# Optimization experiments

Hardware: AMD Instinct MI355X
Metric: run time of the kernel (lower is better)

## Reference

```python
import jax, jax.numpy as jnp
import numpy as np

LOG_2PI = float(np.log(2.0 * np.pi))
LOSS_BETA = 1.0
SIGMA = 1.0
EPS = 1e-6


def setup_inputs() -> dict:
    key = jax.random.key(0)
    z_activations = jax.random.normal(key, (2048, 16, 8), dtype=jnp.float32)
    return {"z_activations": z_activations}


def reference(z_activations):
    N, num_attr, pose_dim = z_activations.shape
    x = z_activations.reshape(N, -1)  # (N, K)
    K = x.shape[1]

    # standardize (torch.std is unbiased, ddof=1)
    mean = jnp.mean(x, axis=0, keepdims=True)
    std = jnp.std(x, axis=0, keepdims=True, ddof=1)
    x = (x - mean) / (std + EPS)

    logN = jnp.log(jnp.asarray(N, dtype=x.dtype))

    # per-dimension pairwise squared differences: (N, N, K)
    d = (x[:, None, :] - x[None, :, :]) ** 2

    # joint: log p(x_i | x_j) for K-dim Gaussian, sigma=1
    sq_dist = jnp.sum(d, axis=2)  # (N, N)
    c_joint = -0.5 * K * LOG_2PI - K * jnp.log(jnp.asarray(SIGMA, dtype=x.dtype))
    log_prob_joint = c_joint - sq_dist / (2.0 * SIGMA ** 2)
    log_q_z_given_x = jax.nn.logsumexp(log_prob_joint, axis=1) - logN  # (N,)

    # marginals: 1-D Gaussian per dim, all K at once (fuses the torch K-loop)
    c_marg = -0.5 * LOG_2PI - jnp.log(jnp.asarray(SIGMA, dtype=x.dtype))
    log_prob_marg = c_marg - d / (2.0 * SIGMA ** 2)  # (N, N, K)
    log_q_z_j = jax.nn.logsumexp(log_prob_marg, axis=1) - logN  # (N, K)
    sum_log_q_z_j = jnp.sum(log_q_z_j, axis=1)  # (N,)

    tc_loss = jnp.mean(log_q_z_given_x - sum_log_q_z_j)
    return tc_loss * LOSS_BETA
```

## Files before the change

### kernel.cpp

```cpp
#include <hip/hip_runtime.h>

#define NROWS 2048
#define KDIM  128
#define TJ    64
#define NCELL 16
#define PORD  10

typedef float v4f __attribute__((ext_vector_type(4)));

__device__ __forceinline__ float fexp2(float x){ return __builtin_amdgcn_exp2f(x); }
__device__ __forceinline__ float flog2(float x){ return __builtin_amdgcn_logf(x); }

#define CS 0.8493218002880191f

template<int CTRL>
__device__ __forceinline__ float dpp_ror(float v){
  int r = __builtin_amdgcn_update_dpp(0, __builtin_bit_cast(int, v), CTRL, 0xF, 0xF, true);
  return __builtin_bit_cast(float, r);
}

__device__ __forceinline__ void col_stats(const float* __restrict__ accum, int k,
                                          float& scale, float& shift){
  float s = accum[k], s2 = accum[KDIM + k];
  float m = s * (1.f / NROWS);
  float var = fmaxf((s2 - (float)NROWS * m * m) * (1.f / (NROWS - 1)), 0.f);
  scale = 1.f / (sqrtf(var) + 1e-6f);
  shift = -m * scale;
}

__device__ __forceinline__ void quad_stats(const float* __restrict__ accum, int q,
                                           float4& sc, float4& sh){
  const float4 s  = reinterpret_cast<const float4*>(accum)[q];
  const float4 s2 = reinterpret_cast<const float4*>(accum + KDIM)[q];
  const float invN = 1.f / NROWS, invN1 = 1.f / (NROWS - 1);
#define COMP(c) { float m = s.c * invN; \
                  float var = fmaxf((s2.c - (float)NROWS * m * m) * invN1, 0.f); \
                  float sca = CS / (sqrtf(var) + 1e-6f); sc.c = sca; sh.c = -m * sca; }
  COMP(x) COMP(y) COMP(z) COMP(w)
#undef COMP
}

__global__ __launch_bounds__(1024) void tc_stats(const float* __restrict__ x,
                                                 float* __restrict__ accum){
  const int t  = threadIdx.x;
  const int k  = t & 127;
  const int rg = t >> 7;
  const int r0 = blockIdx.x * 64;
  float s = 0.f, s2 = 0.f;
  #pragma unroll
  for (int it = 0; it < 8; ++it){
    float v = x[(size_t)(r0 + it * 8 + rg) * KDIM + k];
    s += v;
    s2 = fmaf(v, v, s2);
  }
  __shared__ float ls[8][128], ls2[8][128];
  ls[rg][k] = s; ls2[rg][k] = s2;
  __syncthreads();
  if (t < 128){
    float a = 0.f, b = 0.f;
    #pragma unroll
    for (int g = 0; g < 8; ++g){ a += ls[g][t]; b += ls2[g][t]; }
    atomicAdd(&accum[t], a);
    atomicAdd(&accum[128 + t], b);
  }
}

__global__ __launch_bounds__(128) void tc_moments(const float* __restrict__ x,
                                                  const float* __restrict__ accum,
                                                  float* __restrict__ mom2){
  const int k   = blockIdx.x >> 4;
  const int seg = blockIdx.x & 15;
  const int t   = threadIdx.x;
  __shared__ float lm[NCELL * PORD];
  lm[t] = 0.f;
  if (t < 32) lm[128 + t] = 0.f;
  __syncthreads();

  float scale, shift; col_stats(accum, k, scale, shift);
  const int row = seg * 128 + t;
  float y = fmaf(x[(size_t)row * KDIM + k], scale, shift);
  int c = (int)floorf(y * 2.f + 8.f);
  c = min(max(c, 0), NCELL - 1);
  float u = y - (-3.75f + 0.5f * (float)c);
  float* b10 = &lm[c * PORD];
  atomicAdd(&b10[0], 1.f);
  float pw = u;
  atomicAdd(&b10[1], pw);
  pw *= u; atomicAdd(&b10[2], pw * 0.5f);
  pw *= u; atomicAdd(&b10[3], pw * 1.6666666666e-1f);
  pw *= u; atomicAdd(&b10[4], pw * 4.1666666666e-2f);
  pw *= u; atomicAdd(&b10[5], pw * 8.3333333333e-3f);
  pw *= u; atomicAdd(&b10[6], pw * 1.3888888889e-3f);
  pw *= u; atomicAdd(&b10[7], pw * 1.9841269841e-4f);
  pw *= u; atomicAdd(&b10[8], pw * 2.4801587302e-5f);
  pw *= u; atomicAdd(&b10[9], pw * 2.7557319224e-6f);
  __syncthreads();

  for (int idx = t; idx < NCELL * PORD; idx += 128){
    int c2 = idx / PORD, m = idx - c2 * PORD;
    atomicAdd(&mom2[(size_t)(c2 * KDIM + k) * 12 + m], lm[idx]);
  }
}

__global__ __launch_bounds__(256) void tc_eval(const float* __restrict__ x,
                                               const float* __restrict__ accum,
                                               const float* __restrict__ mom2,
                                               float* __restrict__ slog){
  const int t   = threadIdx.x;
  const int k   = t & 127;
  const int ir  = t >> 7;
  const int row = blockIdx.x * 2 + ir;
  float scale, shift; col_stats(accum, k, scale, shift);
  const float y = fmaf(x[(size_t)row * KDIM + k], scale, shift);

  float S = 0.f;
  #pragma unroll
  for (int c = 0; c < NCELL; ++c){
    const float* mp = mom2 + (size_t)(c * KDIM + k) * 12;
    float4 q0 = *reinterpret_cast<const float4*>(mp);
    float4 q1 = *reinterpret_cast<const float4*>(mp + 4);
    float4 q2 = *reinterpret_cast<const float4*>(mp + 8);
    float s  = y - (-3.75f + 0.5f * (float)c);
    float sc = s * CS;
    float e  = fexp2(-(sc * sc));
    float prev = 1.f, cur = s, nxt;
    float inner = fmaf(q0.y, s, q0.x);
    nxt = fmaf(s, cur, -prev);        inner = fmaf(q0.z, nxt, inner); prev = cur; cur = nxt;
    nxt = fmaf(s, cur, -2.f * prev);  inner = fmaf(q0.w, nxt, inner); prev = cur; cur = nxt;
    nxt = fmaf(s, cur, -3.f * prev);  inner = fmaf(q1.x, nxt, inner); prev = cur; cur = nxt;
    nxt = fmaf(s, cur, -4.f * prev);  inner = fmaf(q1.y, nxt, inner); prev = cur; cur = nxt;
    nxt = fmaf(s, cur, -5.f * prev);  inner = fmaf(q1.z, nxt, inner); prev = cur; cur = nxt;
    nxt = fmaf(s, cur, -6.f * prev);  inner = fmaf(q1.w, nxt, inner); prev = cur; cur = nxt;
    nxt = fmaf(s, cur, -7.f * prev);  inner = fmaf(q2.x, nxt, inner); prev = cur; cur = nxt;
    nxt = fmaf(s, cur, -8.f * prev);  inner = fmaf(q2.y, nxt, inner);
    S = fmaf(e, inner, S);
  }
  float lg = flog2(S);
  #pragma unroll
  for (int off = 1; off < 64; off <<= 1) lg += __shfl_xor(lg, off);
  if ((t & 63) == 0) atomicAdd(&slog[row], lg);
}

__global__ __launch_bounds__(512) void tc_joint(const float* __restrict__ x,
                                                const float* __restrict__ accum,
                                                float* __restrict__ joint){
  __shared__ float tile[TJ][KDIM];
  const int t    = threadIdx.x;
  const int wave = t >> 6;
  const int lane = t & 63;
  const int g    = lane >> 4;
  const int h    = lane & 15;
  const int row  = blockIdx.x * 32 + wave * 4 + g;
  const int jbase = blockIdx.y * 256;

  const int kq = t & 31;
  float4 sc4, sh4; quad_stats(accum, kq, sc4, sh4);

  v4f xA, xB;
  {
    float4 scA, shA, scB, shB;
    quad_stats(accum, h,      scA, shA);
    quad_stats(accum, 16 + h, scB, shB);
    float4 rA = reinterpret_cast<const float4*>(x + (size_t)row * KDIM)[h];
    float4 rB = reinterpret_cast<const float4*>(x + (size_t)row * KDIM)[16 + h];
    xA = (v4f){fmaf(rA.x, scA.x, shA.x), fmaf(rA.y, scA.y, shA.y),
               fmaf(rA.z, scA.z, shA.z), fmaf(rA.w, scA.w, shA.w)};
    xB = (v4f){fmaf(rB.x, scB.x, shB.x), fmaf(rB.y, scB.y, shB.y),
               fmaf(rB.z, scB.z, shB.z), fmaf(rB.w, scB.w, shB.w)};
  }

  float jacc = 0.f;
  const int jr0 = t >> 5;

  for (int jt = 0; jt < 256; jt += TJ){
    __syncthreads();
    #pragma unroll
    for (int p = 0; p < 4; ++p){
      const int jr = jr0 + 16 * p;
      float4 v = reinterpret_cast<const float4*>(x + (size_t)(jbase + jt + jr) * KDIM)[kq];
      v4f w = {fmaf(v.x, sc4.x, sh4.x), fmaf(v.y, sc4.y, sh4.y),
               fmaf(v.z, sc4.z, sh4.z), fmaf(v.w, sc4.w, sh4.w)};
      *reinterpret_cast<v4f*>(&tile[jr][kq * 4]) = w;
    }
    __syncthreads();

    #pragma unroll 8
    for (int j = 0; j < TJ; ++j){
      const v4f a = *reinterpret_cast<const v4f*>(&tile[j][4 * h]);
      const v4f b = *reinterpret_cast<const v4f*>(&tile[j][64 + 4 * h]);
      v4f uA = xA - a, uB = xB - b;
      float pd = uA.x * uA.x;
      pd = fmaf(uA.y, uA.y, pd); pd = fmaf(uA.z, uA.z, pd); pd = fmaf(uA.w, uA.w, pd);
      pd = fmaf(uB.x, uB.x, pd); pd = fmaf(uB.y, uB.y, pd);
      pd = fmaf(uB.z, uB.z, pd); pd = fmaf(uB.w, uB.w, pd);
      pd += dpp_ror<0x121>(pd);
      pd += dpp_ror<0x122>(pd);
      pd += dpp_ror<0x124>(pd);
      pd += dpp_ror<0x128>(pd);
      if (__ballot(pd < 65.f)) jacc += fexp2(-pd);
    }
  }
  if (h == 0) atomicAdd(&joint[row], jacc);
}

__global__ __launch_bounds__(256) void tc_final(const float* __restrict__ joint,
                                                const float* __restrict__ slog,
                                                float* __restrict__ out){
  const int r = blockIdx.x * 256 + threadIdx.x;
  float vi = 0.6931471805599453f * (flog2(joint[r]) - slog[r]) + 968.32661124224364f;
  #pragma unroll
  for (int off = 32; off > 0; off >>= 1) vi += __shfl_down(vi, off);
  __shared__ float rs[4];
  const int wave = threadIdx.x >> 6, lane = threadIdx.x & 63;
  if (lane == 0) rs[wave] = vi;
  __syncthreads();
  if (threadIdx.x == 0){
    float tot = rs[0] + rs[1] + rs[2] + rs[3];
    atomicAdd(out, tot * (1.0f / NROWS));
  }
}

extern "C" void kernel_launch(void* const* d_in, const int* in_sizes, int n_in,
                              void* d_out, int out_size, void* d_ws, size_t ws_size,
                              hipStream_t stream){
  const float* x = (const float*)d_in[0];
  float* out   = (float*)d_out;
  float* wsf   = (float*)d_ws;
  float* accum = wsf;
  float* joint = wsf + 256;
  float* slog  = wsf + 256 + 2048;
  float* mom2  = wsf + 256 + 4096;
  const size_t ws_floats = 256 + 4096 + 24576;
  (void)hipMemsetAsync(wsf, 0, ws_floats * sizeof(float), stream);
  (void)hipMemsetAsync(d_out, 0, sizeof(float), stream);

  tc_stats  <<<32, 1024, 0, stream>>>(x, accum);
  tc_moments<<<KDIM * 16, 128, 0, stream>>>(x, accum, mom2);
  tc_joint  <<<dim3(64, 8), 512, 0, stream>>>(x, accum, joint);
  tc_eval   <<<NROWS / 2, 256, 0, stream>>>(x, accum, mom2, slog);
  tc_final  <<<NROWS / 256, 256, 0, stream>>>(joint, slog, out);
}
```

Baseline: 131.9 us.

## Exploit pairwise symmetry in joint kernel and fuse eval/final into it

The joint kernel now visits only the upper-triangular 256x256 block pairs. Off-diagonal tiles also add their exponentials into the column rows through shared-memory atomics, which roughly halves the pairwise work. The marginal-evaluation and final-reduction kernels are folded into the joint kernel, and a last-block counter performs the final sum. The two memsets are replaced by zeroing inside tc_stats, and the global atomics for column stats become per-block partials that tc_moments reduces. The costs are extra shared atomics in the hot loop, load imbalance between diagonal and off-diagonal blocks, and a fixed-order serial tail.

```diff
diff --git a/kernel.cpp b/kernel.cpp
--- a/kernel.cpp
+++ b/kernel.cpp
@@ -5,6 +5,7 @@
 #define TJ    64
 #define NCELL 16
 #define PORD  10
+#define NJBLK 576
 
 typedef float v4f __attribute__((ext_vector_type(4)));
 
@@ -19,9 +20,16 @@
   return __builtin_bit_cast(float, r);
 }
 
-__device__ __forceinline__ void col_stats(const float* __restrict__ accum, int k,
-                                          float& scale, float& shift){
-  float s = accum[k], s2 = accum[KDIM + k];
+#define OFF_PART   0
+#define OFF_ACCUM  8192
+#define OFF_JOINT  8448
+#define OFF_SLOG   10496
+#define OFF_MOM    12544
+#define OFF_CTR    33024
+#define ZERO_BASE  OFF_JOINT
+#define ZERO_LEN   (2048 + 2048 + 20480 + 4)
+
+__device__ __forceinline__ void col_stats_from(float s, float s2, float& scale, float& shift){
   float m = s * (1.f / NROWS);
   float var = fmaxf((s2 - (float)NROWS * m * m) * (1.f / (NROWS - 1)), 0.f);
   scale = 1.f / (sqrtf(var) + 1e-6f);
@@ -41,11 +49,15 @@
 }
 
 __global__ __launch_bounds__(1024) void tc_stats(const float* __restrict__ x,
-                                                 float* __restrict__ accum){
+                                                 float* __restrict__ ws){
   const int t  = threadIdx.x;
   const int k  = t & 127;
   const int rg = t >> 7;
   const int r0 = blockIdx.x * 64;
+  {
+    int idx = blockIdx.x * 1024 + t;
+    if (idx < ZERO_LEN) ws[ZERO_BASE + idx] = 0.f;
+  }
   float s = 0.f, s2 = 0.f;
   #pragma unroll
   for (int it = 0; it < 8; ++it){
@@ -60,23 +72,33 @@
     float a = 0.f, b = 0.f;
     #pragma unroll
     for (int g = 0; g < 8; ++g){ a += ls[g][t]; b += ls2[g][t]; }
-    atomicAdd(&accum[t], a);
-    atomicAdd(&accum[128 + t], b);
+    ws[OFF_PART + blockIdx.x * 256 + t]       = a;
+    ws[OFF_PART + blockIdx.x * 256 + 128 + t] = b;
   }
 }
 
 __global__ __launch_bounds__(128) void tc_moments(const float* __restrict__ x,
-                                                  const float* __restrict__ accum,
-                                                  float* __restrict__ mom2){
+                                                  float* __restrict__ ws){
   const int k   = blockIdx.x >> 4;
   const int seg = blockIdx.x & 15;
   const int t   = threadIdx.x;
   __shared__ float lm[NCELL * PORD];
   lm[t] = 0.f;
   if (t < 32) lm[128 + t] = 0.f;
-  __syncthreads();
-
-  float scale, shift; col_stats(accum, k, scale, shift);
+
+  float s = 0.f, s2 = 0.f;
+  #pragma unroll
+  for (int b = 0; b < 32; ++b){
+    s  += ws[OFF_PART + b * 256 + k];
+    s2 += ws[OFF_PART + b * 256 + 128 + k];
+  }
+  if (seg == 0 && t == 0){
+    ws[OFF_ACCUM + k]       = s;
+    ws[OFF_ACCUM + 128 + k] = s2;
+  }
+  float scale, shift; col_stats_from(s, s2, scale, shift);
+  __syncthreads();
+
   const int row = seg * 128 + t;
   float y = fmaf(x[(size_t)row * KDIM + k], scale, shift);
   int c = (int)floorf(y * 2.f + 8.f);
@@ -96,62 +118,42 @@
   pw *= u; atomicAdd(&b10[9], pw * 2.7557319224e-6f);
   __syncthreads();
 
+  float* mom = ws + OFF_MOM;
   for (int idx = t; idx < NCELL * PORD; idx += 128){
     int c2 = idx / PORD, m = idx - c2 * PORD;
-    atomicAdd(&mom2[(size_t)(c2 * KDIM + k) * 12 + m], lm[idx]);
-  }
-}
-
-__global__ __launch_bounds__(256) void tc_eval(const float* __restrict__ x,
-                                               const float* __restrict__ accum,
-                                               const float* __restrict__ mom2,
-                                               float* __restrict__ slog){
-  const int t   = threadIdx.x;
-  const int k   = t & 127;
-  const int ir  = t >> 7;
-  const int row = blockIdx.x * 2 + ir;
-  float scale, shift; col_stats(accum, k, scale, shift);
-  const float y = fmaf(x[(size_t)row * KDIM + k], scale, shift);
-
-  float S = 0.f;
-  #pragma unroll
-  for (int c = 0; c < NCELL; ++c){
-    const float* mp = mom2 + (size_t)(c * KDIM + k) * 12;
-    float4 q0 = *reinterpret_cast<const float4*>(mp);
-    float4 q1 = *reinterpret_cast<const float4*>(mp + 4);
-    float4 q2 = *reinterpret_cast<const float4*>(mp + 8);
-    float s  = y - (-3.75f + 0.5f * (float)c);
-    float sc = s * CS;
-    float e  = fexp2(-(sc * sc));
-    float prev = 1.f, cur = s, nxt;
-    float inner = fmaf(q0.y, s, q0.x);
-    nxt = fmaf(s, cur, -prev);        inner = fmaf(q0.z, nxt, inner); prev = cur; cur = nxt;
-    nxt = fmaf(s, cur, -2.f * prev);  inner = fmaf(q0.w, nxt, inner); prev = cur; cur = nxt;
-    nxt = fmaf(s, cur, -3.f * prev);  inner = fmaf(q1.x, nxt, inner); prev = cur; cur = nxt;
-    nxt = fmaf(s, cur, -4.f * prev);  inner = fmaf(q1.y, nxt, inner); prev = cur; cur = nxt;
-    nxt = fmaf(s, cur, -5.f * prev);  inner = fmaf(q1.z, nxt, inner); prev = cur; cur = nxt;
-    nxt = fmaf(s, cur, -6.f * prev);  inner = fmaf(q1.w, nxt, inner); prev = cur; cur = nxt;
-    nxt = fmaf(s, cur, -7.f * prev);  inner = fmaf(q2.x, nxt, inner); prev = cur; cur = nxt;
-    nxt = fmaf(s, cur, -8.f * prev);  inner = fmaf(q2.y, nxt, inner);
-    S = fmaf(e, inner, S);
-  }
-  float lg = flog2(S);
-  #pragma unroll
-  for (int off = 1; off < 64; off <<= 1) lg += __shfl_xor(lg, off);
-  if ((t & 63) == 0) atomicAdd(&slog[row], lg);
+    atomicAdd(&mom[(size_t)(c2 * KDIM + k) * PORD + m], lm[idx]);
+  }
 }
 
 __global__ __launch_bounds__(512) void tc_joint(const float* __restrict__ x,
-                                                const float* __restrict__ accum,
-                                                float* __restrict__ joint){
+                                                float* __restrict__ ws,
+                                                float* __restrict__ out){
   __shared__ float tile[TJ][KDIM];
+  __shared__ float colacc[128];
+  __shared__ int   lastflag;
+  const float* accum = ws + OFF_ACCUM;
+  float* joint = ws + OFF_JOINT;
+  float* slog  = ws + OFF_SLOG;
+  const float* mom = ws + OFF_MOM;
+
+  const int bid  = blockIdx.x;
   const int t    = threadIdx.x;
   const int wave = t >> 6;
   const int lane = t & 63;
   const int g    = lane >> 4;
   const int h    = lane & 15;
-  const int row  = blockIdx.x * 32 + wave * 4 + g;
-  const int jbase = blockIdx.y * 256;
+
+  int pair = bid >> 4, sub = (bid >> 1) & 7, jhalf = bid & 1;
+  int a = 0, rem = pair;
+  while (rem >= 8 - a){ rem -= 8 - a; ++a; }
+  const int b = a + rem;
+  const int i0 = a * 256 + sub * 32;
+  const int j0 = b * 256 + jhalf * 128;
+  const bool offdiag = (a != b);
+
+  const int row = i0 + wave * 4 + g;
+
+  if (t < 128) colacc[t] = 0.f;
 
   const int kq = t & 31;
   float4 sc4, sh4; quad_stats(accum, kq, sc4, sh4);
@@ -172,12 +174,12 @@
   float jacc = 0.f;
   const int jr0 = t >> 5;
 
-  for (int jt = 0; jt < 256; jt += TJ){
+  for (int jt = 0; jt < 128; jt += TJ){
     __syncthreads();
     #pragma unroll
     for (int p = 0; p < 4; ++p){
       const int jr = jr0 + 16 * p;
-      float4 v = reinterpret_cast<const float4*>(x + (size_t)(jbase + jt + jr) * KDIM)[kq];
+      float4 v = reinterpret_cast<const float4*>(x + (size_t)(j0 + jt + jr) * KDIM)[kq];
       v4f w = {fmaf(v.x, sc4.x, sh4.x), fmaf(v.y, sc4.y, sh4.y),
                fmaf(v.z, sc4.z, sh4.z), fmaf(v.w, sc4.w, sh4.w)};
       *reinterpret_cast<v4f*>(&tile[jr][kq * 4]) = w;
@@ -186,37 +188,95 @@
 
     #pragma unroll 8
     for (int j = 0; j < TJ; ++j){
-      const v4f a = *reinterpret_cast<const v4f*>(&tile[j][4 * h]);
-      const v4f b = *reinterpret_cast<const v4f*>(&tile[j][64 + 4 * h]);
-      v4f uA = xA - a, uB = xB - b;
-      float pd = uA.x * uA.x;
-      pd = fmaf(uA.y, uA.y, pd); pd = fmaf(uA.z, uA.z, pd); pd = fmaf(uA.w, uA.w, pd);
-      pd = fmaf(uB.x, uB.x, pd); pd = fmaf(uB.y, uB.y, pd);
-      pd = fmaf(uB.z, uB.z, pd); pd = fmaf(uB.w, uB.w, pd);
+      const v4f aa = *reinterpret_cast<const v4f*>(&tile[j][4 * h]);
+      const v4f bb = *reinterpret_cast<const v4f*>(&tile[j][64 + 4 * h]);
+      v4f uA = xA - aa, uB = xB - bb;
+      float p0 = uA.x * uA.x, p1 = uA.y * uA.y;
+      p0 = fmaf(uA.z, uA.z, p0); p1 = fmaf(uA.w, uA.w, p1);
+      p0 = fmaf(uB.x, uB.x, p0); p1 = fmaf(uB.y, uB.y, p1);
+      p0 = fmaf(uB.z, uB.z, p0); p1 = fmaf(uB.w, uB.w, p1);
+      float pd = p0 + p1;
       pd += dpp_ror<0x121>(pd);
       pd += dpp_ror<0x122>(pd);
       pd += dpp_ror<0x124>(pd);
       pd += dpp_ror<0x128>(pd);
-      if (__ballot(pd < 65.f)) jacc += fexp2(-pd);
-    }
-  }
+      if (__ballot(pd < 65.f)){
+        float e = fexp2(-pd);
+        jacc += e;
+        if (offdiag && h == 0) atomicAdd(&colacc[jt + j], e);
+      }
+    }
+  }
+
   if (h == 0) atomicAdd(&joint[row], jacc);
-}
-
-__global__ __launch_bounds__(256) void tc_final(const float* __restrict__ joint,
-                                                const float* __restrict__ slog,
-                                                float* __restrict__ out){
-  const int r = blockIdx.x * 256 + threadIdx.x;
-  float vi = 0.6931471805599453f * (flog2(joint[r]) - slog[r]) + 968.32661124224364f;
-  #pragma unroll
-  for (int off = 32; off > 0; off >>= 1) vi += __shfl_down(vi, off);
-  __shared__ float rs[4];
-  const int wave = threadIdx.x >> 6, lane = threadIdx.x & 63;
-  if (lane == 0) rs[wave] = vi;
-  __syncthreads();
-  if (threadIdx.x == 0){
-    float tot = rs[0] + rs[1] + rs[2] + rs[3];
-    atomicAdd(out, tot * (1.0f / NROWS));
+  __syncthreads();
+  if (offdiag && t < 128){
+    float c = colacc[t];
+    if (c != 0.f) atomicAdd(&joint[j0 + t], c);
+  }
+
+  if (bid < 512){
+    const int k  = t & 127;
+    const int ir = t >> 7;
+    const int r  = bid * 4 + ir;
+    float scale, shift;
+    col_stats_from(accum[k], accum[128 + k], scale, shift);
+    const float y = fmaf(x[(size_t)r * KDIM + k], scale, shift);
+    float S = 0.f;
+    #pragma unroll
+    for (int c = 0; c < NCELL; ++c){
+      const float* mp = mom + (size_t)(c * KDIM + k) * PORD;
+      float q0 = mp[0], q1 = mp[1], q2 = mp[2], q3 = mp[3], q4 = mp[4];
+      float q5 = mp[5], q6 = mp[6], q7 = mp[7], q8 = mp[8], q9 = mp[9];
+      float s  = y - (-3.75f + 0.5f * (float)c);
+      float scl = s * CS;
+      float e  = fexp2(-(scl * scl));
+      float prev = 1.f, cur = s, nxt;
+      float inner = fmaf(q1, s, q0);
+      nxt = fmaf(s, cur, -prev);        inner = fmaf(q2, nxt, inner); prev = cur; cur = nxt;
+      nxt = fmaf(s, cur, -2.f * prev);  inner = fmaf(q3, nxt, inner); prev = cur; cur = nxt;
+      nxt = fmaf(s, cur, -3.f * prev);  inner = fmaf(q4, nxt, inner); prev = cur; cur = nxt;
+      nxt = fmaf(s, cur, -4.f * prev);  inner = fmaf(q5, nxt, inner); prev = cur; cur = nxt;
+      nxt = fmaf(s, cur, -5.f * prev);  inner = fmaf(q6, nxt, inner); prev = cur; cur = nxt;
+      nxt = fmaf(s, cur, -6.f * prev);  inner = fmaf(q7, nxt, inner); prev = cur; cur = nxt;
+      nxt = fmaf(s, cur, -7.f * prev);  inner = fmaf(q8, nxt, inner); prev = cur; cur = nxt;
+      nxt = fmaf(s, cur, -8.f * prev);  inner = fmaf(q9, nxt, inner);
+      S = fmaf(e, inner, S);
+    }
+    float lg = flog2(S);
+    #pragma unroll
+    for (int off = 1; off < 64; off <<= 1) lg += __shfl_xor(lg, off);
+    if (lane == 0) atomicAdd(&slog[r], lg);
+  }
+
+  __syncthreads();
+  if (t == 0){
+    __threadfence();
+    unsigned int* ctr = (unsigned int*)(ws + OFF_CTR);
+    unsigned int old = __hip_atomic_fetch_add(ctr, 1u, __ATOMIC_ACQ_REL, __HIP_MEMORY_SCOPE_AGENT);
+    lastflag = (old == NJBLK - 1);
+  }
+  __syncthreads();
+  if (lastflag){
+    __shared__ float red[8];
+    float acc = 0.f;
+    #pragma unroll
+    for (int q = 0; q < 4; ++q){
+      int r = q * 512 + t;
+      float jv = __hip_atomic_load(&joint[r], __ATOMIC_RELAXED, __HIP_MEMORY_SCOPE_AGENT);
+      float sv = __hip_atomic_load(&slog[r],  __ATOMIC_RELAXED, __HIP_MEMORY_SCOPE_AGENT);
+      acc += 0.6931471805599453f * (flog2(jv) - sv);
+    }
+    #pragma unroll
+    for (int off = 1; off < 64; off <<= 1) acc += __shfl_xor(acc, off);
+    if (lane == 0) red[wave] = acc;
+    __syncthreads();
+    if (t == 0){
+      float tot = 0.f;
+      #pragma unroll
+      for (int w2 = 0; w2 < 8; ++w2) tot += red[w2];
+      out[0] = tot * (1.0f / NROWS) + 968.32661124224364f;
+    }
   }
 }
 
@@ -224,19 +284,10 @@
                               void* d_out, int out_size, void* d_ws, size_t ws_size,
                               hipStream_t stream){
   const float* x = (const float*)d_in[0];
-  float* out   = (float*)d_out;
-  float* wsf   = (float*)d_ws;
-  float* accum = wsf;
-  float* joint = wsf + 256;
-  float* slog  = wsf + 256 + 2048;
-  float* mom2  = wsf + 256 + 4096;
-  const size_t ws_floats = 256 + 4096 + 24576;
-  (void)hipMemsetAsync(wsf, 0, ws_floats * sizeof(float), stream);
-  (void)hipMemsetAsync(d_out, 0, sizeof(float), stream);
-
-  tc_stats  <<<32, 1024, 0, stream>>>(x, accum);
-  tc_moments<<<KDIM * 16, 128, 0, stream>>>(x, accum, mom2);
-  tc_joint  <<<dim3(64, 8), 512, 0, stream>>>(x, accum, joint);
-  tc_eval   <<<NROWS / 2, 256, 0, stream>>>(x, accum, mom2, slog);
-  tc_final  <<<NROWS / 256, 256, 0, stream>>>(joint, slog, out);
-}
+  float* out = (float*)d_out;
+  float* ws  = (float*)d_ws;
+
+  tc_stats  <<<32, 1024, 0, stream>>>(x, ws);
+  tc_moments<<<KDIM * 16, 128, 0, stream>>>(x, ws);
+  tc_joint  <<<NJBLK, 512, 0, stream>>>(x, ws, out);
+}
```

Result: faster. 116.4 us (-11.8%).
